# Kernel tuning notes

Measured on AMD Instinct MI355X. Metric: run time of the kernel, lower is better.

Reference implementation:

```python
import jax, jax.numpy as jnp
import numpy as np

N = 50000      # nodes
E = 800000     # edges (before self-loops)
IN = 128       # in_channels
C = 64         # hidden_channels (per head)
H = 2          # heads
OUT = 40       # out_channels (classes)
SLOPE = 0.2    # PyG GATConv leaky_relu negative_slope


def setup_inputs() -> dict:
    key = jax.random.key(0)
    ks = jax.random.split(key, 12)
    def glorot(k, shape, fan):
        return (jax.random.normal(k, shape, jnp.float32) / np.float32(np.sqrt(fan)))
    x = jax.random.normal(ks[0], (N, IN), jnp.float32)
    edge_index = jax.random.randint(ks[1], (2, E), 0, N, dtype=jnp.int32)
    return {
        "x": x,
        "edge_index": edge_index,
        "W0": glorot(ks[2], (IN, H * C), IN),
        "a_src0": glorot(ks[3], (H, C), C),
        "a_dst0": glorot(ks[4], (H, C), C),
        "b0": jnp.zeros((H * C,), jnp.float32),
        "W1": glorot(ks[5], (H * C, H * C), H * C),
        "a_src1": glorot(ks[6], (H, C), C),
        "a_dst1": glorot(ks[7], (H, C), C),
        "b1": jnp.zeros((H * C,), jnp.float32),
        "lin_w": glorot(ks[8], (H * C * 2, OUT), H * C * 2),
        "lin_b": jnp.zeros((OUT,), jnp.float32),
    }


def gat_conv(x, W, a_src, a_dst, b, src, dst):
    # x: [N, F_in] -> h: [N, H, C]
    h = (x @ W).reshape(-1, H, C)
    # per-node attention logits (PyG splits a into src/dst halves)
    es = jnp.einsum("nhc,hc->nh", h, a_src)  # [N, H]
    ed = jnp.einsum("nhc,hc->nh", h, a_dst)  # [N, H]
    e = jax.nn.leaky_relu(es[src] + ed[dst], SLOPE)  # [Etot, H]
    # segment softmax over incoming edges of each destination node
    m = jax.ops.segment_max(e, dst, num_segments=N)          # [N, H]
    m = jnp.where(jnp.isneginf(m), 0.0, m)
    w = jnp.exp(e - m[dst])                                  # [Etot, H]
    denom = jax.ops.segment_sum(w, dst, num_segments=N)      # [N, H]
    alpha = w / jnp.maximum(denom[dst], 1e-16)               # [Etot, H]
    # scatter-aggregate messages: [Etot, H, C] -> [N, H, C]
    out = jax.ops.segment_sum(alpha[:, :, None] * h[src], dst, num_segments=N)
    return out.reshape(-1, H * C) + b  # concat=True over heads


def reference(x, edge_index, W0, a_src0, a_dst0, b0, W1, a_src1, a_dst1, b1, lin_w, lin_b):
    # PyG GATConv adds self-loops by default
    loops = jnp.arange(N, dtype=edge_index.dtype)
    src = jnp.concatenate([edge_index[0], loops])
    dst = jnp.concatenate([edge_index[1], loops])
    h1 = jax.nn.elu(gat_conv(x, W0, a_src0, a_dst0, b0, src, dst))   # [N, H*C]
    h2 = jax.nn.elu(gat_conv(h1, W1, a_src1, a_dst1, b1, src, dst))  # [N, H*C]
    h_cat = jnp.concatenate([h1, h2], axis=1)                        # [N, 2*H*C]
    logits = h_cat @ lin_w + lin_b                                   # [N, OUT]
    return jax.nn.log_softmax(logits, axis=1)
```

## Files before the change

### kernel.cpp

```cpp
#include <hip/hip_runtime.h>
#include <hip/hip_fp16.h>
#include <math.h>

#define NN 50000
#define E0 800000
#define ET 850000
#define NBX 200
#define NBK 196
#define TILE 4096
#define NTILES 208
#define CAP 8192

typedef unsigned int uint32;
typedef unsigned short u16;
typedef __attribute__((ext_vector_type(8))) _Float16 f16x8;
typedef __attribute__((ext_vector_type(4))) float f32x4;

__device__ __forceinline__ u16 f2h(float f) {
  return __half_as_ushort(__float2half(f));
}
__device__ __forceinline__ float h2f(u16 u) {
  return __half2float(__ushort_as_half(u));
}

__global__ __launch_bounds__(256) void partition_prep_kernel(
    const int* __restrict__ ei, int* __restrict__ gcursor, uint32* __restrict__ packed,
    const float* __restrict__ x, const float* __restrict__ W0, const float* __restrict__ W1,
    const float* __restrict__ lw,
    u16* __restrict__ xb, u16* __restrict__ w0t, u16* __restrict__ w1t, u16* __restrict__ lwt)
{
  __shared__ __align__(16) char smem[23872];
  const int b = blockIdx.x;
  const int tid = threadIdx.x;
  if (b < NTILES) {
    int* hist = (int*)smem;
    int* s    = (int*)(smem + 784);
    int* scanb = (int*)(smem + 1808);
    int* gofs  = (int*)(smem + 2592);
    uint32* shuf = (uint32*)(smem + 3376);
    unsigned char* sbkt = (unsigned char*)(smem + 19760);
    const int t0 = b * TILE;
    for (int i = tid; i < NBK; i += 256) hist[i] = 0;
    __syncthreads();
    int myb[16]; int myr[16]; uint32 mypk[16];
#pragma unroll
    for (int i = 0; i < 16; ++i) {
      int e = t0 + i * 256 + tid;
      myb[i] = -1;
      if (e < ET) {
        int src, dst;
        if (e < E0) { src = ei[e]; dst = ei[E0 + e]; }
        else        { src = e - E0; dst = src; }
        myb[i] = dst >> 8;
        mypk[i] = ((uint32)(dst & 255) << 16) | (uint32)src;
        myr[i] = atomicAdd(&hist[myb[i]], 1);
      }
    }
    __syncthreads();
    int v = (tid < NBK) ? hist[tid] : 0;
    int val = v;
    s[tid] = val;
    __syncthreads();
#pragma unroll
    for (int off = 1; off < 256; off <<= 1) {
      int t = (tid >= off) ? s[tid - off] : 0;
      __syncthreads();
      val += t;
      s[tid] = val;
      __syncthreads();
    }
    if (tid < NBK) {
      scanb[tid] = val - v;
      gofs[tid] = (v > 0) ? atomicAdd(&gcursor[tid], v) : 0;
    }
    __syncthreads();
#pragma unroll
    for (int i = 0; i < 16; ++i) {
      if (myb[i] >= 0) {
        int slot = scanb[myb[i]] + myr[i];
        shuf[slot] = mypk[i];
        sbkt[slot] = (unsigned char)myb[i];
      }
    }
    __syncthreads();
    const int tcount = (t0 + TILE <= ET) ? TILE : (ET - t0);
    for (int i = tid; i < tcount; i += 256) {
      int bb = sbkt[i];
      packed[(size_t)bb * CAP + gofs[bb] + (i - scanb[bb])] = shuf[i];
    }
  } else {
    const int b2 = b - NTILES;
    if (b2 < NBX) {
      const float4* x4 = (const float4*)x;
      ushort4* xb4 = (ushort4*)xb;
      const int total = NN * 128 / 4;
      for (int i = b2 * 256 + tid; i < total; i += NBX * 256) {
        float4 v = x4[i];
        ushort4 u;
        u.x = f2h(v.x); u.y = f2h(v.y); u.z = f2h(v.z); u.w = f2h(v.w);
        xb4[i] = u;
      }
    } else if (b2 < NBX + 2) {
      const float* W = (b2 == NBX) ? W0 : W1;
      u16* Wt = (b2 == NBX) ? w0t : w1t;
      float (*tile)[129] = (float(*)[129])smem;
      for (int k0 = 0; k0 < 128; k0 += 32) {
        __syncthreads();
#pragma unroll
        for (int it = 0; it < 4; ++it) {
          int q = tid + it * 256;
          int kk = q >> 5, n4 = (q & 31) * 4;
          float4 v = *(const float4*)&W[(k0 + kk) * 128 + n4];
          tile[kk][n4 + 0] = v.x; tile[kk][n4 + 1] = v.y;
          tile[kk][n4 + 2] = v.z; tile[kk][n4 + 3] = v.w;
        }
        __syncthreads();
        int n = tid >> 1, h = (tid & 1) * 16;
        __align__(16) u16 tmp[16];
#pragma unroll
        for (int j = 0; j < 16; ++j) tmp[j] = f2h(tile[h + j][n]);
        *(uint4*)&Wt[n * 128 + k0 + h] = *(uint4*)&tmp[0];
        *(uint4*)&Wt[n * 128 + k0 + h + 8] = *(uint4*)&tmp[8];
      }
    } else {
      for (int idx = tid; idx < 48 * 256; idx += 256) {
        int j = idx >> 8, k = idx & 255;
        lwt[idx] = (j < 40) ? f2h(lw[k * 40 + j]) : (u16)0;
      }
    }
  }
}

__global__ __launch_bounds__(256) void build_kernel(
    const uint32* __restrict__ packed, const int* __restrict__ gcursor,
    int2* __restrict__ rowinfo, int* __restrict__ csr_src)
{
  __shared__ int h[256];
  __shared__ int s[256];
  __shared__ int sc[256];
  __shared__ int cur[256];
  __shared__ int ptot_s;
  __shared__ u16 simg[CAP];
  const int b = blockIdx.x;
  const int tid = threadIdx.x;
  const int cnt = gcursor[b];
  const uint32* pk = packed + (size_t)b * CAP;
  h[tid] = 0;
  cur[tid] = 0;
  __syncthreads();
  for (int i = tid; i < cnt; i += 256) atomicAdd(&h[(pk[i] >> 16) & 255], 1);
  __syncthreads();
  const int pd = (h[tid] + 7) & ~7;
  int val = pd;
  s[tid] = val;
  __syncthreads();
#pragma unroll
  for (int off = 1; off < 256; off <<= 1) {
    int t = (tid >= off) ? s[tid - off] : 0;
    __syncthreads();
    val += t;
    s[tid] = val;
    __syncthreads();
  }
  sc[tid] = val - pd;
  if (tid == 255) ptot_s = val;
  __syncthreads();
  const int ptot = ptot_s;
  for (int i = tid; i < ptot; i += 256) simg[i] = (u16)NN;
  __syncthreads();
  for (int i = tid; i < cnt; i += 256) {
    uint32 p = pk[i];
    int dl = (p >> 16) & 255;
    int r = atomicAdd(&cur[dl], 1);
    simg[sc[dl] + r] = (u16)(p & 0xFFFFu);
  }
  __syncthreads();
  int n = b * 256 + tid;
  if (n < NN) rowinfo[n] = make_int2(b * CAP + sc[tid], pd);
  for (int i = tid; i < ptot; i += 256) csr_src[b * CAP + i] = (int)simg[i];
}

__global__ __launch_bounds__(256) void gemm_att_kernel(
    const u16* __restrict__ Xb, const u16* __restrict__ Wt,
    const float* __restrict__ avs, const float* __restrict__ avd,
    u16* __restrict__ hfeat, float* __restrict__ es, float* __restrict__ ed,
    int nnodes)
{
  __shared__ u16 hout[64 * 136];
  __shared__ float es_s[2][64];
  __shared__ float ed_s[2][64];
  const int tid = threadIdx.x;
  const int wid = tid >> 6, lane = tid & 63;
  const int quad = lane >> 4, lc = lane & 15;
  const int n0 = blockIdx.x * 64;
  if (blockIdx.x == 0 && tid < 2) es[2 * NN + tid] = -1e30f;

  const int arow = wid * 16 + lc;
  const int rrow = min(n0 + arow, nnodes - 1);

  f32x4 acc[8];
#pragma unroll
  for (int t = 0; t < 8; ++t) acc[t] = (f32x4){0.f, 0.f, 0.f, 0.f};
#pragma unroll
  for (int ks = 0; ks < 4; ++ks) {
    const int k0 = ks * 32 + quad * 8;
    f16x8 a = *(const f16x8*)&Xb[(size_t)rrow * 128 + k0];
#pragma unroll
    for (int t = 0; t < 8; ++t) {
      f16x8 b = *(const f16x8*)&Wt[(t * 16 + lc) * 128 + k0];
      acc[t] = __builtin_amdgcn_mfma_f32_16x16x32_f16(a, b, acc[t], 0, 0, 0);
    }
  }

  float av_s[8], av_d[8];
#pragma unroll
  for (int t = 0; t < 8; ++t) { av_s[t] = avs[t * 16 + lc]; av_d[t] = avd[t * 16 + lc]; }
#pragma unroll
  for (int r = 0; r < 4; ++r) {
    float s0 = 0.f, s1 = 0.f, d0 = 0.f, d1 = 0.f;
#pragma unroll
    for (int t = 0; t < 4; ++t) { s0 += acc[t][r] * av_s[t]; d0 += acc[t][r] * av_d[t]; }
#pragma unroll
    for (int t = 4; t < 8; ++t) { s1 += acc[t][r] * av_s[t]; d1 += acc[t][r] * av_d[t]; }
#pragma unroll
    for (int m = 1; m < 16; m <<= 1) {
      s0 += __shfl_xor(s0, m); s1 += __shfl_xor(s1, m);
      d0 += __shfl_xor(d0, m); d1 += __shfl_xor(d1, m);
    }
    if (lc == 0) {
      int row = wid * 16 + quad * 4 + r;
      es_s[0][row] = s0; es_s[1][row] = s1;
      ed_s[0][row] = d0; ed_s[1][row] = d1;
    }
  }
#pragma unroll
  for (int t = 0; t < 8; ++t)
#pragma unroll
    for (int r = 0; r < 4; ++r)
      hout[(wid * 16 + quad * 4 + r) * 136 + t * 16 + lc] = f2h(acc[t][r]);
  __syncthreads();
#pragma unroll
  for (int it = 0; it < 4; ++it) {
    int g = tid + it * 256;
    int r = g >> 4, c8 = (g & 15) * 8;
    if (n0 + r < nnodes)
      *(uint4*)&hfeat[(size_t)(n0 + r) * 128 + c8] = *(const uint4*)&hout[r * 136 + c8];
  }
  if (tid < 64) {
    int n = n0 + tid;
    if (n < nnodes) {
      es[n * 2 + 0] = es_s[0][tid]; es[n * 2 + 1] = es_s[1][tid];
      ed[n * 2 + 0] = ed_s[0][tid]; ed[n * 2 + 1] = ed_s[1][tid];
    }
  }
}

__global__ __launch_bounds__(256) void aggregate_kernel(
    const uint4* __restrict__ hfeat4, const float* __restrict__ es, const float* __restrict__ ed,
    const int2* __restrict__ rowinfo, const int* __restrict__ csr_src,
    const float* __restrict__ bias, u16* __restrict__ out, int nnodes)
{
  int n = (blockIdx.x * blockDim.x + threadIdx.x) >> 6;
  int lane = threadIdx.x & 63;
  if (n >= nnodes) return;
  const int eg = lane >> 4;
  const int fl = lane & 15;
  const int hd = (fl >= 8) ? 1 : 0;
  const int2 ri = rowinfo[n];
  const int nch = ri.y >> 3;
  const int j0 = ri.x + eg;
  const float edn = ed[n * 2 + hd];

  float acc[8];
#pragma unroll
  for (int t = 0; t < 8; ++t) acc[t] = 0.f;
  float den = 0.f;

  int i0A = csr_src[j0], i1A = csr_src[j0 + 4];
  float e0 = es[i0A * 2 + hd] + edn; e0 = fmaxf(e0, 0.2f * e0);
  float e1 = es[i1A * 2 + hd] + edn; e1 = fmaxf(e1, 0.2f * e1);
  float w0A = __expf(e0), w1A = __expf(e1);
  for (int c = 0;;) {
    uint4 h0 = hfeat4[(size_t)i0A * 16 + fl];
    uint4 h1 = hfeat4[(size_t)i1A * 16 + fl];
    bool more = (c + 1 < nch);
    int i0B, i1B; float w0B, w1B;
    if (more) {
      int jb = j0 + (c + 1) * 8;
      i0B = csr_src[jb]; i1B = csr_src[jb + 4];
      float f0 = es[i0B * 2 + hd] + edn; f0 = fmaxf(f0, 0.2f * f0);
      float f1 = es[i1B * 2 + hd] + edn; f1 = fmaxf(f1, 0.2f * f1);
      w0B = __expf(f0); w1B = __expf(f1);
    }
    acc[0] = fmaf(w0A, h2f((u16)(h0.x & 0xFFFFu)), acc[0]);
    acc[1] = fmaf(w0A, h2f((u16)(h0.x >> 16)),     acc[1]);
    acc[2] = fmaf(w0A, h2f((u16)(h0.y & 0xFFFFu)), acc[2]);
    acc[3] = fmaf(w0A, h2f((u16)(h0.y >> 16)),     acc[3]);
    acc[4] = fmaf(w0A, h2f((u16)(h0.z & 0xFFFFu)), acc[4]);
    acc[5] = fmaf(w0A, h2f((u16)(h0.z >> 16)),     acc[5]);
    acc[6] = fmaf(w0A, h2f((u16)(h0.w & 0xFFFFu)), acc[6]);
    acc[7] = fmaf(w0A, h2f((u16)(h0.w >> 16)),     acc[7]);
    acc[0] = fmaf(w1A, h2f((u16)(h1.x & 0xFFFFu)), acc[0]);
    acc[1] = fmaf(w1A, h2f((u16)(h1.x >> 16)),     acc[1]);
    acc[2] = fmaf(w1A, h2f((u16)(h1.y & 0xFFFFu)), acc[2]);
    acc[3] = fmaf(w1A, h2f((u16)(h1.y >> 16)),     acc[3]);
    acc[4] = fmaf(w1A, h2f((u16)(h1.z & 0xFFFFu)), acc[4]);
    acc[5] = fmaf(w1A, h2f((u16)(h1.z >> 16)),     acc[5]);
    acc[6] = fmaf(w1A, h2f((u16)(h1.w & 0xFFFFu)), acc[6]);
    acc[7] = fmaf(w1A, h2f((u16)(h1.w >> 16)),     acc[7]);
    den += w0A + w1A;
    if (!more) break;
    i0A = i0B; i1A = i1B; w0A = w0B; w1A = w1B;
    ++c;
  }

#pragma unroll
  for (int t = 0; t < 8; ++t) {
    acc[t] += __shfl_xor(acc[t], 16);
    acc[t] += __shfl_xor(acc[t], 32);
  }
  den += __shfl_xor(den, 16);
  den += __shfl_xor(den, 32);

  if (eg == 0) {
    float inv = 1.f / den;
    float4 b0 = *(const float4*)&bias[fl * 8];
    float4 b1 = *(const float4*)&bias[fl * 8 + 4];
    float bv[8] = {b0.x, b0.y, b0.z, b0.w, b1.x, b1.y, b1.z, b1.w};
    u16 pk[8];
#pragma unroll
    for (int t = 0; t < 8; ++t) {
      float v = acc[t] * inv + bv[t];
      v = (v > 0.f) ? v : (__expf(v) - 1.f);
      pk[t] = f2h(v);
    }
    uint4 o;
    o.x = (uint32)pk[0] | ((uint32)pk[1] << 16);
    o.y = (uint32)pk[2] | ((uint32)pk[3] << 16);
    o.z = (uint32)pk[4] | ((uint32)pk[5] << 16);
    o.w = (uint32)pk[6] | ((uint32)pk[7] << 16);
    ((uint4*)out)[(size_t)n * 16 + fl] = o;
  }
}

__global__ __launch_bounds__(256) void final_kernel(
    const u16* __restrict__ h1b, const u16* __restrict__ h2b,
    const u16* __restrict__ lwt, const float* __restrict__ lb,
    float* __restrict__ out, int nnodes)
{
  const int tid = threadIdx.x;
  const int wid = tid >> 6, lane = tid & 63;
  const int quad = lane >> 4, lc = lane & 15;
  const int n0 = blockIdx.x * 64;
  const int arow = wid * 16 + lc;
  const int rrow = min(n0 + arow, nnodes - 1);

  f32x4 acc[3];
#pragma unroll
  for (int t = 0; t < 3; ++t) acc[t] = (f32x4){0.f, 0.f, 0.f, 0.f};
#pragma unroll
  for (int ks = 0; ks < 8; ++ks) {
    const u16* hsrc = (ks < 4) ? h1b : h2b;
    const int k0 = (ks & 3) * 32 + quad * 8;
    const int kl = ks * 32 + quad * 8;
    f16x8 a = *(const f16x8*)&hsrc[(size_t)rrow * 128 + k0];
#pragma unroll
    for (int t = 0; t < 3; ++t) {
      f16x8 b = *(const f16x8*)&lwt[(t * 16 + lc) * 256 + kl];
      acc[t] = __builtin_amdgcn_mfma_f32_16x16x32_f16(a, b, acc[t], 0, 0, 0);
    }
  }

  float bv[3];
  bool valid[3];
#pragma unroll
  for (int t = 0; t < 3; ++t) {
    int col = t * 16 + lc;
    valid[t] = (col < 40);
    bv[t] = valid[t] ? lb[col] : 0.f;
  }
#pragma unroll
  for (int r = 0; r < 4; ++r) {
    int row = wid * 16 + quad * 4 + r;
    int n = n0 + row;
    float v[3];
    float mx = -INFINITY;
#pragma unroll
    for (int t = 0; t < 3; ++t) {
      v[t] = acc[t][r] + bv[t];
      if (valid[t]) mx = fmaxf(mx, v[t]);
    }
    mx = fmaxf(mx, __shfl_xor(mx, 1));
    mx = fmaxf(mx, __shfl_xor(mx, 2));
    mx = fmaxf(mx, __shfl_xor(mx, 4));
    mx = fmaxf(mx, __shfl_xor(mx, 8));
    float s = 0.f;
#pragma unroll
    for (int t = 0; t < 3; ++t) if (valid[t]) s += __expf(v[t] - mx);
    s += __shfl_xor(s, 1);
    s += __shfl_xor(s, 2);
    s += __shfl_xor(s, 4);
    s += __shfl_xor(s, 8);
    float lg = mx + __logf(s);
    if (n < nnodes) {
#pragma unroll
      for (int t = 0; t < 3; ++t)
        if (valid[t]) out[(size_t)n * 40 + t * 16 + lc] = v[t] - lg;
    }
  }
}


extern "C" void kernel_launch(void* const* d_in, const int* in_sizes, int n_in,
                              void* d_out, int out_size, void* d_ws, size_t ws_size,
                              hipStream_t stream) {
  const float* x   = (const float*)d_in[0];
  const int*   ei  = (const int*)d_in[1];
  const float* W0  = (const float*)d_in[2];
  const float* as0 = (const float*)d_in[3];
  const float* ad0 = (const float*)d_in[4];
  const float* b0  = (const float*)d_in[5];
  const float* W1  = (const float*)d_in[6];
  const float* as1 = (const float*)d_in[7];
  const float* ad1 = (const float*)d_in[8];
  const float* b1  = (const float*)d_in[9];
  const float* lw  = (const float*)d_in[10];
  const float* lb  = (const float*)d_in[11];
  float* out = (float*)d_out;

  char* p = (char*)d_ws;
  auto carve = [&](size_t bytes) { char* r = p; p += (bytes + 255) & ~(size_t)255; return r; };
  u16* xb     = (u16*)carve((size_t)NN * 128 * 2);
  u16* w0t    = (u16*)carve(128 * 128 * 2);
  u16* w1t    = (u16*)carve(128 * 128 * 2);
  u16* lwt    = (u16*)carve(48 * 256 * 2);
  u16* hfeat  = (u16*)carve((size_t)(NN + 1) * 128 * 2);
  u16* h1b    = (u16*)carve((size_t)NN * 128 * 2);
  u16* h2b    = (u16*)carve((size_t)NN * 128 * 2);
  float* es   = (float*)carve((size_t)(NN + 1) * 2 * 4);
  float* ed   = (float*)carve((size_t)NN * 2 * 4);
  int2* rowinfo = (int2*)carve((size_t)NN * 8);
  int* csr    = (int*)carve((size_t)NBK * CAP * 4);
  uint32* packed = (uint32*)carve((size_t)NBK * CAP * 4);
  int* gcursor = (int*)carve(NBK * 4);

  hipMemsetAsync(gcursor, 0, NBK * 4, stream);

  partition_prep_kernel<<<NTILES + NBX + 3, 256, 0, stream>>>(
      ei, gcursor, packed, x, W0, W1, lw, xb, w0t, w1t, lwt);
  build_kernel<<<NBK, 256, 0, stream>>>(packed, gcursor, rowinfo, csr);

  gemm_att_kernel<<<(NN + 63) / 64, 256, 0, stream>>>(xb, w0t, as0, ad0, hfeat, es, ed, NN);
  aggregate_kernel<<<(NN * 64 + 255) / 256, 256, 0, stream>>>((const uint4*)hfeat, es, ed, rowinfo, csr, b0, h1b, NN);
  gemm_att_kernel<<<(NN + 63) / 64, 256, 0, stream>>>(h1b, w1t, as1, ad1, hfeat, es, ed, NN);
  aggregate_kernel<<<(NN * 64 + 255) / 256, 256, 0, stream>>>((const uint4*)hfeat, es, ed, rowinfo, csr, b1, h2b, NN);
  final_kernel<<<(NN + 63) / 64, 256, 0, stream>>>(h1b, h2b, lwt, lb, out, NN);
}
```

Measured before the change: 247.8 us.

## Fuse CSR build into first GEMM launch and convert x to fp16 inline

```diff
diff --git a/kernel.cpp b/kernel.cpp
--- a/kernel.cpp
+++ b/kernel.cpp
@@ -5,7 +5,6 @@
 #define NN 50000
 #define E0 800000
 #define ET 850000
-#define NBX 200
 #define NBK 196
 #define TILE 4096
 #define NTILES 208
@@ -25,9 +24,9 @@
 
 __global__ __launch_bounds__(256) void partition_prep_kernel(
     const int* __restrict__ ei, int* __restrict__ gcursor, uint32* __restrict__ packed,
-    const float* __restrict__ x, const float* __restrict__ W0, const float* __restrict__ W1,
+    const float* __restrict__ W0, const float* __restrict__ W1,
     const float* __restrict__ lw,
-    u16* __restrict__ xb, u16* __restrict__ w0t, u16* __restrict__ w1t, u16* __restrict__ lwt)
+    u16* __restrict__ w0t, u16* __restrict__ w1t, u16* __restrict__ lwt)
 {
   __shared__ __align__(16) char smem[23872];
   const int b = blockIdx.x;
@@ -88,60 +87,47 @@
       int bb = sbkt[i];
       packed[(size_t)bb * CAP + gofs[bb] + (i - scanb[bb])] = shuf[i];
     }
+  } else if (b < NTILES + 2) {
+    const float* W = (b == NTILES) ? W0 : W1;
+    u16* Wt = (b == NTILES) ? w0t : w1t;
+    float (*tile)[129] = (float(*)[129])smem;
+    for (int k0 = 0; k0 < 128; k0 += 32) {
+      __syncthreads();
+#pragma unroll
+      for (int it = 0; it < 4; ++it) {
+        int q = tid + it * 256;
+        int kk = q >> 5, n4 = (q & 31) * 4;
+        float4 v = *(const float4*)&W[(k0 + kk) * 128 + n4];
+        tile[kk][n4 + 0] = v.x; tile[kk][n4 + 1] = v.y;
+        tile[kk][n4 + 2] = v.z; tile[kk][n4 + 3] = v.w;
+      }
+      __syncthreads();
+      int n = tid >> 1, h = (tid & 1) * 16;
+      __align__(16) u16 tmp[16];
+#pragma unroll
+      for (int j = 0; j < 16; ++j) tmp[j] = f2h(tile[h + j][n]);
+      *(uint4*)&Wt[n * 128 + k0 + h] = *(uint4*)&tmp[0];
+      *(uint4*)&Wt[n * 128 + k0 + h + 8] = *(uint4*)&tmp[8];
+    }
   } else {
-    const int b2 = b - NTILES;
-    if (b2 < NBX) {
-      const float4* x4 = (const float4*)x;
-      ushort4* xb4 = (ushort4*)xb;
-      const int total = NN * 128 / 4;
-      for (int i = b2 * 256 + tid; i < total; i += NBX * 256) {
-        float4 v = x4[i];
-        ushort4 u;
-        u.x = f2h(v.x); u.y = f2h(v.y); u.z = f2h(v.z); u.w = f2h(v.w);
-        xb4[i] = u;
-      }
-    } else if (b2 < NBX + 2) {
-      const float* W = (b2 == NBX) ? W0 : W1;
-      u16* Wt = (b2 == NBX) ? w0t : w1t;
-      float (*tile)[129] = (float(*)[129])smem;
-      for (int k0 = 0; k0 < 128; k0 += 32) {
-        __syncthreads();
-#pragma unroll
-        for (int it = 0; it < 4; ++it) {
-          int q = tid + it * 256;
-          int kk = q >> 5, n4 = (q & 31) * 4;
-          float4 v = *(const float4*)&W[(k0 + kk) * 128 + n4];
-          tile[kk][n4 + 0] = v.x; tile[kk][n4 + 1] = v.y;
-          tile[kk][n4 + 2] = v.z; tile[kk][n4 + 3] = v.w;
-        }
-        __syncthreads();
-        int n = tid >> 1, h = (tid & 1) * 16;
-        __align__(16) u16 tmp[16];
-#pragma unroll
-        for (int j = 0; j < 16; ++j) tmp[j] = f2h(tile[h + j][n]);
-        *(uint4*)&Wt[n * 128 + k0 + h] = *(uint4*)&tmp[0];
-        *(uint4*)&Wt[n * 128 + k0 + h + 8] = *(uint4*)&tmp[8];
-      }
-    } else {
-      for (int idx = tid; idx < 48 * 256; idx += 256) {
-        int j = idx >> 8, k = idx & 255;
-        lwt[idx] = (j < 40) ? f2h(lw[k * 40 + j]) : (u16)0;
-      }
-    }
-  }
-}
-
-__global__ __launch_bounds__(256) void build_kernel(
+    for (int idx = tid; idx < 48 * 256; idx += 256) {
+      int j = idx >> 8, k = idx & 255;
+      lwt[idx] = (j < 40) ? f2h(lw[k * 40 + j]) : (u16)0;
+    }
+  }
+}
+
+__device__ __forceinline__ void build_body(
+    char* smem, int b,
     const uint32* __restrict__ packed, const int* __restrict__ gcursor,
-    int2* __restrict__ rowinfo, int* __restrict__ csr_src)
+    int2* __restrict__ rowinfo, u16* __restrict__ csr_src)
 {
-  __shared__ int h[256];
-  __shared__ int s[256];
-  __shared__ int sc[256];
-  __shared__ int cur[256];
-  __shared__ int ptot_s;
-  __shared__ u16 simg[CAP];
-  const int b = blockIdx.x;
+  int* h      = (int*)smem;
+  int* s      = (int*)(smem + 1024);
+  int* sc     = (int*)(smem + 2048);
+  int* cur    = (int*)(smem + 3072);
+  int* ptot_p = (int*)(smem + 4096);
+  u16* simg   = (u16*)(smem + 4112);
   const int tid = threadIdx.x;
   const int cnt = gcursor[b];
   const uint32* pk = packed + (size_t)b * CAP;
@@ -163,9 +149,9 @@
     __syncthreads();
   }
   sc[tid] = val - pd;
-  if (tid == 255) ptot_s = val;
-  __syncthreads();
-  const int ptot = ptot_s;
+  if (tid == 255) *ptot_p = val;
+  __syncthreads();
+  const int ptot = *ptot_p;
   for (int i = tid; i < ptot; i += 256) simg[i] = (u16)NN;
   __syncthreads();
   for (int i = tid; i < cnt; i += 256) {
@@ -177,18 +163,29 @@
   __syncthreads();
   int n = b * 256 + tid;
   if (n < NN) rowinfo[n] = make_int2(b * CAP + sc[tid], pd);
-  for (int i = tid; i < ptot; i += 256) csr_src[b * CAP + i] = (int)simg[i];
+  uint32* dst = (uint32*)(csr_src + (size_t)b * CAP);
+  const uint32* sim32 = (const uint32*)simg;
+  for (int i = tid; i < (ptot >> 1); i += 256) dst[i] = sim32[i];
 }
 
 __global__ __launch_bounds__(256) void gemm_att_kernel(
-    const u16* __restrict__ Xb, const u16* __restrict__ Wt,
+    const float* __restrict__ Xf, const u16* __restrict__ Xh,
+    const u16* __restrict__ Wt,
     const float* __restrict__ avs, const float* __restrict__ avd,
     u16* __restrict__ hfeat, float* __restrict__ es, float* __restrict__ ed,
-    int nnodes)
+    int nnodes,
+    const uint32* __restrict__ packed, const int* __restrict__ gcursor,
+    int2* __restrict__ rowinfo, u16* __restrict__ csr_src)
 {
-  __shared__ u16 hout[64 * 136];
-  __shared__ float es_s[2][64];
-  __shared__ float ed_s[2][64];
+  __shared__ __align__(16) char smem[20608];
+  const int ngemm = (nnodes + 63) >> 6;
+  if ((int)blockIdx.x >= ngemm) {
+    build_body(smem, (int)blockIdx.x - ngemm, packed, gcursor, rowinfo, csr_src);
+    return;
+  }
+  u16* hout   = (u16*)smem;
+  float* es_s = (float*)(smem + 17408);
+  float* ed_s = (float*)(smem + 17920);
   const int tid = threadIdx.x;
   const int wid = tid >> 6, lane = tid & 63;
   const int quad = lane >> 4, lc = lane & 15;
@@ -204,11 +201,21 @@
 #pragma unroll
   for (int ks = 0; ks < 4; ++ks) {
     const int k0 = ks * 32 + quad * 8;
-    f16x8 a = *(const f16x8*)&Xb[(size_t)rrow * 128 + k0];
+    f16x8 a;
+    if (Xf) {
+      const float4* xr = (const float4*)&Xf[(size_t)rrow * 128 + k0];
+      float4 v0 = xr[0], v1 = xr[1];
+      a[0] = (_Float16)v0.x; a[1] = (_Float16)v0.y;
+      a[2] = (_Float16)v0.z; a[3] = (_Float16)v0.w;
+      a[4] = (_Float16)v1.x; a[5] = (_Float16)v1.y;
+      a[6] = (_Float16)v1.z; a[7] = (_Float16)v1.w;
+    } else {
+      a = *(const f16x8*)&Xh[(size_t)rrow * 128 + k0];
+    }
 #pragma unroll
     for (int t = 0; t < 8; ++t) {
-      f16x8 b = *(const f16x8*)&Wt[(t * 16 + lc) * 128 + k0];
-      acc[t] = __builtin_amdgcn_mfma_f32_16x16x32_f16(a, b, acc[t], 0, 0, 0);
+      f16x8 bfr = *(const f16x8*)&Wt[(t * 16 + lc) * 128 + k0];
+      acc[t] = __builtin_amdgcn_mfma_f32_16x16x32_f16(a, bfr, acc[t], 0, 0, 0);
     }
   }
 
@@ -229,8 +236,8 @@
     }
     if (lc == 0) {
       int row = wid * 16 + quad * 4 + r;
-      es_s[0][row] = s0; es_s[1][row] = s1;
-      ed_s[0][row] = d0; ed_s[1][row] = d1;
+      es_s[row] = s0; es_s[64 + row] = s1;
+      ed_s[row] = d0; ed_s[64 + row] = d1;
     }
   }
 #pragma unroll
@@ -249,15 +256,15 @@
   if (tid < 64) {
     int n = n0 + tid;
     if (n < nnodes) {
-      es[n * 2 + 0] = es_s[0][tid]; es[n * 2 + 1] = es_s[1][tid];
-      ed[n * 2 + 0] = ed_s[0][tid]; ed[n * 2 + 1] = ed_s[1][tid];
+      es[n * 2 + 0] = es_s[tid];      es[n * 2 + 1] = es_s[64 + tid];
+      ed[n * 2 + 0] = ed_s[tid];      ed[n * 2 + 1] = ed_s[64 + tid];
     }
   }
 }
 
 __global__ __launch_bounds__(256) void aggregate_kernel(
     const uint4* __restrict__ hfeat4, const float* __restrict__ es, const float* __restrict__ ed,
-    const int2* __restrict__ rowinfo, const int* __restrict__ csr_src,
+    const int2* __restrict__ rowinfo, const u16* __restrict__ csr_src,
     const float* __restrict__ bias, u16* __restrict__ out, int nnodes)
 {
   int n = (blockIdx.x * blockDim.x + threadIdx.x) >> 6;
@@ -430,7 +437,6 @@
 
   char* p = (char*)d_ws;
   auto carve = [&](size_t bytes) { char* r = p; p += (bytes + 255) & ~(size_t)255; return r; };
-  u16* xb     = (u16*)carve((size_t)NN * 128 * 2);
   u16* w0t    = (u16*)carve(128 * 128 * 2);
   u16* w1t    = (u16*)carve(128 * 128 * 2);
   u16* lwt    = (u16*)carve(48 * 256 * 2);
@@ -440,19 +446,26 @@
   float* es   = (float*)carve((size_t)(NN + 1) * 2 * 4);
   float* ed   = (float*)carve((size_t)NN * 2 * 4);
   int2* rowinfo = (int2*)carve((size_t)NN * 8);
-  int* csr    = (int*)carve((size_t)NBK * CAP * 4);
+  u16* csr    = (u16*)carve((size_t)NBK * CAP * 2);
   uint32* packed = (uint32*)carve((size_t)NBK * CAP * 4);
   int* gcursor = (int*)carve(NBK * 4);
 
   hipMemsetAsync(gcursor, 0, NBK * 4, stream);
 
-  partition_prep_kernel<<<NTILES + NBX + 3, 256, 0, stream>>>(
-      ei, gcursor, packed, x, W0, W1, lw, xb, w0t, w1t, lwt);
-  build_kernel<<<NBK, 256, 0, stream>>>(packed, gcursor, rowinfo, csr);
-
-  gemm_att_kernel<<<(NN + 63) / 64, 256, 0, stream>>>(xb, w0t, as0, ad0, hfeat, es, ed, NN);
-  aggregate_kernel<<<(NN * 64 + 255) / 256, 256, 0, stream>>>((const uint4*)hfeat, es, ed, rowinfo, csr, b0, h1b, NN);
-  gemm_att_kernel<<<(NN + 63) / 64, 256, 0, stream>>>(h1b, w1t, as1, ad1, hfeat, es, ed, NN);
-  aggregate_kernel<<<(NN * 64 + 255) / 256, 256, 0, stream>>>((const uint4*)hfeat, es, ed, rowinfo, csr, b1, h2b, NN);
-  final_kernel<<<(NN + 63) / 64, 256, 0, stream>>>(h1b, h2b, lwt, lb, out, NN);
-}
+  const int NG = (NN + 63) / 64;
+
+  partition_prep_kernel<<<NTILES + 3, 256, 0, stream>>>(
+      ei, gcursor, packed, W0, W1, lw, w0t, w1t, lwt);
+
+  gemm_att_kernel<<<NG + NBK, 256, 0, stream>>>(
+      x, nullptr, w0t, as0, ad0, hfeat, es, ed, NN, packed, gcursor, rowinfo, csr);
+  aggregate_kernel<<<(NN * 64 + 255) / 256, 256, 0, stream>>>(
+      (const uint4*)hfeat, es, ed, rowinfo, csr, b0, h1b, NN);
+
+  gemm_att_kernel<<<NG, 256, 0, stream>>>(
+      nullptr, h1b, w1t, as1, ad1, hfeat, es, ed, NN, packed, gcursor, rowinfo, csr);
+  aggregate_kernel<<<(NN * 64 + 255) / 256, 256, 0, stream>>>(
+      (const uint4*)hfeat, es, ed, rowinfo, csr, b1, h2b, NN);
+
+  final_kernel<<<NG, 256, 0, stream>>>(h1b, h2b, lwt, lb, out, NN);
+}
```

Result: faster. 238.4 us (-3.8%).
